# Performance work log

Hardware: AMD Instinct MI355X
Metric: run time of the kernel (lower is better)

## Reference

```python
import jax, jax.numpy as jnp
import numpy as np

IN, H, B, T, OUT = 128, 512, 256, 512, 2

def _lstm_layer(x, Wih, Whh, bih, bhh):
    # x: [B, T, D_in] -> h_seq: [B, T, H]. PyTorch gate order: i, f, g, o.
    gx = jnp.einsum('btd,gd->btg', x, Wih) + bih + bhh  # [B, T, 4H]
    gx = jnp.transpose(gx, (1, 0, 2))                    # [T, B, 4H]
    Hh = Whh.shape[1]
    def step(carry, g_t):
        h, c = carry
        g = g_t + h @ Whh.T
        i = jax.nn.sigmoid(g[:, 0*Hh:1*Hh])
        f = jax.nn.sigmoid(g[:, 1*Hh:2*Hh])
        gg = jnp.tanh(g[:, 2*Hh:3*Hh])
        o = jax.nn.sigmoid(g[:, 3*Hh:4*Hh])
        c = f * c + i * gg
        h = o * jnp.tanh(c)
        return (h, c), h
    h0 = jnp.zeros((x.shape[0], Hh), x.dtype)
    (_, _), hs = jax.lax.scan(step, (h0, h0), gx)
    return jnp.transpose(hs, (1, 0, 2))  # [B, T, H]

def setup_inputs() -> dict:
    key = jax.random.key(0)
    ks = jax.random.split(key, 11)
    s = 1.0 / np.sqrt(H)
    u = lambda k, shp: jax.random.uniform(k, shp, jnp.float32, -s, s)
    return {
        'x':    jax.random.normal(ks[0], (B, T, IN), jnp.float32),
        'Wih0': u(ks[1], (4 * H, IN)), 'Whh0': u(ks[2], (4 * H, H)),
        'bih0': u(ks[3], (4 * H,)),    'bhh0': u(ks[4], (4 * H,)),
        'Wih1': u(ks[5], (4 * H, H)),  'Whh1': u(ks[6], (4 * H, H)),
        'bih1': u(ks[7], (4 * H,)),    'bhh1': u(ks[8], (4 * H,)),
        'Wfc':  u(ks[9], (OUT, H)),    'bfc':  u(ks[10], (OUT,)),
    }

def reference(x, Wih0, Whh0, bih0, bhh0, Wih1, Whh1, bih1, bhh1, Wfc, bfc):
    h1 = _lstm_layer(x, Wih0, Whh0, bih0, bhh0)   # layer 0
    h2 = _lstm_layer(h1, Wih1, Whh1, bih1, bhh1)  # layer 1
    return h2[:, -1, :] @ Wfc.T + bfc             # [B, OUT]
```

## Files before the change

kernel.cpp:

```cpp
#include <hip/hip_runtime.h>

#define IN_DIM 128
#define HID    512
#define BATCH  256
#define SEQT   512
#define G4H    2048
#define K0     640
#define K1     1024
#define NC0    20
#define NC1    32
#define ROWB   2048
#define FSTRIDE 32

typedef __attribute__((ext_vector_type(8))) short bf16x8;
typedef __attribute__((ext_vector_type(4))) float f32x4;

#define MFMA16 __builtin_amdgcn_mfma_f32_16x16x32_bf16
#define GL(r, g, c) ((r) * 132 + (g) * 33 + (c))

__device__ __forceinline__ unsigned short f2bf(float f) {
  unsigned u = __float_as_uint(f);
  u += 0x7fffu + ((u >> 16) & 1u);
  return (unsigned short)(u >> 16);
}
__device__ __forceinline__ float bf2f(unsigned short s) {
  return __uint_as_float(((unsigned)s) << 16);
}
__device__ __forceinline__ float sigm(float x) { return 1.0f / (1.0f + __expf(-x)); }
__device__ __forceinline__ float tanh_f(float x) {
  float xc = fminf(fmaxf(x, -15.0f), 15.0f);
  float e = __expf(2.0f * xc);
  return (e - 1.0f) / (e + 1.0f);
}

__device__ __forceinline__ unsigned ald(const unsigned* p) {
  return __hip_atomic_load(p, __ATOMIC_RELAXED, __HIP_MEMORY_SCOPE_AGENT);
}

__global__ void conv_weights(const float* __restrict__ Wih0, const float* __restrict__ Whh0,
                             const float* __restrict__ Wih1, const float* __restrict__ Whh1,
                             const float* __restrict__ bih0, const float* __restrict__ bhh0,
                             const float* __restrict__ bih1, const float* __restrict__ bhh1,
                             short* __restrict__ W0h, short* __restrict__ W0l,
                             short* __restrict__ W1h, short* __restrict__ W1l,
                             float* __restrict__ bsum0, float* __restrict__ bsum1) {
  int idx = blockIdx.x * blockDim.x + threadIdx.x;
  const int N0 = G4H * K0, N1 = G4H * K1;
  if (idx < N0) {
    int tile = idx / (K0 * 16), rem = idx % (K0 * 16);
    int kcg = rem >> 9, l = (rem >> 3) & 63, j = rem & 7;
    int slice = tile >> 2, g = tile & 3;
    int c = l & 15, k = kcg * 32 + ((l >> 4) << 3) + j;
    int n = g * HID + slice * 16 + c;
    float w = (k < IN_DIM) ? Wih0[n * IN_DIM + k] : Whh0[n * HID + (k - IN_DIM)];
    unsigned short hi = f2bf(w);
    W0h[idx] = (short)hi;
    W0l[idx] = (short)f2bf(w - bf2f(hi));
  } else if (idx < N0 + N1) {
    int d = idx - N0;
    int tile = d / (K1 * 16), rem = d % (K1 * 16);
    int kcg = rem >> 9, l = (rem >> 3) & 63, j = rem & 7;
    int slice = tile >> 2, g = tile & 3;
    int c = l & 15, k = kcg * 32 + ((l >> 4) << 3) + j;
    int n = g * HID + slice * 16 + c;
    float w = (k < HID) ? Wih1[n * HID + k] : Whh1[n * HID + (k - HID)];
    unsigned short hi = f2bf(w);
    W1h[d] = (short)hi;
    W1l[d] = (short)f2bf(w - bf2f(hi));
  } else if (idx < N0 + N1 + G4H) {
    int n = idx - (N0 + N1);
    bsum0[n] = bih0[n] + bhh0[n];
  } else if (idx < N0 + N1 + 2 * G4H) {
    int n = idx - (N0 + N1 + G4H);
    bsum1[n] = bih1[n] + bhh1[n];
  }
}


__device__ __forceinline__ void stage_l0(char* Ah, const float* __restrict__ x,
                                         const unsigned short* __restrict__ h0p,
                                         int b0, int s, int tid) {
  const int row = tid >> 5, c32 = tid & 31;
  const int rx = (row & 7) << 4;
  char* base = Ah + row * ROWB;
  {
    const float* xs = x + ((size_t)(b0 + row) * SEQT + s) * IN_DIM + c32 * 4;
    float4 xv = *(const float4*)xs;
    unsigned short h0 = f2bf(xv.x), h1 = f2bf(xv.y), h2 = f2bf(xv.z), h3 = f2bf(xv.w);
    uint2 hd = {(unsigned)h0 | ((unsigned)h1 << 16), (unsigned)h2 | ((unsigned)h3 << 16)};
    uint2 ld = {(unsigned)f2bf(xv.x - bf2f(h0)) | ((unsigned)f2bf(xv.y - bf2f(h1)) << 16),
                (unsigned)f2bf(xv.z - bf2f(h2)) | ((unsigned)f2bf(xv.w - bf2f(h3)) << 16)};
    *(uint2*)(base + ((c32 * 8) ^ rx)) = hd;
    *(uint2*)(base + ((1280 + c32 * 8) ^ rx)) = ld;
  }
  {
    const unsigned short* hp = h0p + (size_t)(b0 + row) * HID + c32 * 16;
    uint4 v0, v1;
    asm volatile(
        "global_load_dwordx4 %0, %2, off sc0 sc1\n\t"
        "global_load_dwordx4 %1, %2, off offset:16 sc0 sc1\n\t"
        "s_waitcnt vmcnt(0)"
        : "=&v"(v0), "=&v"(v1) : "v"(hp) : "memory");
    const int byte0 = 256 + c32 * 32;
    *(int4*)(base + (byte0 ^ rx)) = *(int4*)&v0;
    *(int4*)(base + ((byte0 + 16) ^ rx)) = *(int4*)&v1;
  }
}

__device__ __forceinline__ void stage_l1(char* Ah,
                                         const unsigned short* __restrict__ h0p,
                                         const unsigned short* __restrict__ h2p,
                                         int b0, int tid) {
  const int row = tid >> 5, c32 = tid & 31;
  const int rx = (row & 7) << 4;
  char* base = Ah + row * ROWB;
  const unsigned short* p0 = h0p + (size_t)(b0 + row) * HID + c32 * 16;
  const unsigned short* p2 = h2p + (size_t)(b0 + row) * HID + c32 * 16;
  uint4 v0, v1, w0, w1;
  asm volatile(
      "global_load_dwordx4 %0, %4, off sc0 sc1\n\t"
      "global_load_dwordx4 %1, %4, off offset:16 sc0 sc1\n\t"
      "global_load_dwordx4 %2, %5, off sc0 sc1\n\t"
      "global_load_dwordx4 %3, %5, off offset:16 sc0 sc1\n\t"
      "s_waitcnt vmcnt(0)"
      : "=&v"(v0), "=&v"(v1), "=&v"(w0), "=&v"(w1)
      : "v"(p0), "v"(p2) : "memory");
  const int b0b = c32 * 32;
  *(int4*)(base + (b0b ^ rx)) = *(int4*)&v0;
  *(int4*)(base + ((b0b + 16) ^ rx)) = *(int4*)&v1;
  const int b2b = 1024 + c32 * 32;
  *(int4*)(base + (b2b ^ rx)) = *(int4*)&w0;
  *(int4*)(base + ((b2b + 16) ^ rx)) = *(int4*)&w1;
}

template <int NKC>
__device__ __forceinline__ void gemm_seq(const char* Ah, bool xlo,
                                         const short* __restrict__ Bh0, const short* __restrict__ Bl0,
                                         const short* __restrict__ Bh1, const short* __restrict__ Bl1,
                                         int lane, int aoff,
                                         f32x4& a00, f32x4& a01, f32x4& a10, f32x4& a11) {
  const int row = lane & 15;
  const int ko  = (lane >> 4) * 8;
  const int rx  = (row & 7) << 4;
  const char* pA0 = Ah + row * ROWB;
  const char* pA1 = Ah + (row + 16) * ROWB;
#pragma unroll
  for (int kc = 0; kc < NKC; ++kc) {
    const int k = aoff + kc * 32;
    const int off = ((k + ko) * 2) ^ rx;
    bf16x8 ah0 = *(const bf16x8*)(pA0 + off);
    bf16x8 ah1 = *(const bf16x8*)(pA1 + off);
    bf16x8 bh0 = *(const bf16x8*)(Bh0 + kc * 512 + lane * 8);
    bf16x8 bl0 = *(const bf16x8*)(Bl0 + kc * 512 + lane * 8);
    bf16x8 bh1 = *(const bf16x8*)(Bh1 + kc * 512 + lane * 8);
    bf16x8 bl1 = *(const bf16x8*)(Bl1 + kc * 512 + lane * 8);
    a00 = MFMA16(ah0, bh0, a00, 0, 0, 0);
    a01 = MFMA16(ah1, bh0, a01, 0, 0, 0);
    a00 = MFMA16(ah0, bl0, a00, 0, 0, 0);
    a01 = MFMA16(ah1, bl0, a01, 0, 0, 0);
    a10 = MFMA16(ah0, bh1, a10, 0, 0, 0);
    a11 = MFMA16(ah1, bh1, a11, 0, 0, 0);
    a10 = MFMA16(ah0, bl1, a10, 0, 0, 0);
    a11 = MFMA16(ah1, bl1, a11, 0, 0, 0);
    if (xlo && k < IN_DIM) {
      const int offl = ((1280 + (k + ko) * 2)) ^ rx;
      bf16x8 al0 = *(const bf16x8*)(pA0 + offl);
      bf16x8 al1 = *(const bf16x8*)(pA1 + offl);
      a00 = MFMA16(al0, bh0, a00, 0, 0, 0);
      a01 = MFMA16(al1, bh0, a01, 0, 0, 0);
      a10 = MFMA16(al0, bh1, a10, 0, 0, 0);
      a11 = MFMA16(al1, bh1, a11, 0, 0, 0);
    }
  }
}

__device__ __forceinline__ void finq32(float* glf, int g, int lane,
                                       const f32x4& a00, const f32x4& a01,
                                       const f32x4& a10, const f32x4& a11) {
  const int col = lane & 15;
  const int r0  = (lane >> 4) * 4;
#pragma unroll
  for (int r = 0; r < 4; ++r) {
    atomicAdd(glf + GL(r0 + r, g, col), a00[r]);
    atomicAdd(glf + GL(16 + r0 + r, g, col), a01[r]);
    atomicAdd(glf + GL(r0 + r, g, col + 16), a10[r]);
    atomicAdd(glf + GL(16 + r0 + r, g, col + 16), a11[r]);
  }
}

__device__ __forceinline__ void group_barrier(unsigned* flags, unsigned target,
                                              int tid, int wid) {
  asm volatile("s_waitcnt vmcnt(0)" ::: "memory");
  __syncthreads();
  if (tid < 64) {
    if (tid == 0)
      __hip_atomic_store(flags + wid * FSTRIDE, target,
                         __ATOMIC_RELAXED, __HIP_MEMORY_SCOPE_AGENT);
    const int i = (tid & 31) * FSTRIDE;
    while (true) {
      unsigned v = ald(flags + i);
      if (__all((int)(v >= target))) break;
      __builtin_amdgcn_s_sleep(1);
    }
  }
  __syncthreads();
}

__global__ void __launch_bounds__(1024, 4) lstm_fused(
    const float* __restrict__ x,
    const float* __restrict__ Wfc, const float* __restrict__ bfc,
    const short* __restrict__ W0h, const short* __restrict__ W0l,
    const short* __restrict__ W1h, const short* __restrict__ W1l,
    const float* __restrict__ bsum0, const float* __restrict__ bsum1,
    unsigned short* __restrict__ h0s, unsigned short* __restrict__ h2s,
    unsigned* __restrict__ counters,
    float* __restrict__ out) {
  const int tid  = threadIdx.x;
  const int wv   = tid >> 6;
  const int lane = tid & 63;
  const int wid  = blockIdx.x & 31;
  const int grp  = blockIdx.x >> 5;
  const int role = wid >> 4;
  const int w16  = wid & 15;
  const int hid0 = w16 * 32;
  const int b0   = grp * 32;
  unsigned* flags = counters + grp * (32 * FSTRIDE);

  __shared__ __align__(16) char AhB[32 * ROWB];
  __shared__ float glf[32 * 132];

  const int g  = wv & 3;
  const int kq = wv >> 2;
  const int t0 = (w16 * 2) * 4 + g, t1 = t0 + 4;
  const short *Bh0, *Bl0, *Bh1, *Bl1;
  int aoff;
  if (role == 0) {
    Bh0 = W0h + ((size_t)t0 * NC0 + (size_t)kq * 5) * 512;
    Bl0 = W0l + ((size_t)t0 * NC0 + (size_t)kq * 5) * 512;
    Bh1 = W0h + ((size_t)t1 * NC0 + (size_t)kq * 5) * 512;
    Bl1 = W0l + ((size_t)t1 * NC0 + (size_t)kq * 5) * 512;
    aoff = kq * 160;
  } else {
    Bh0 = W1h + ((size_t)t0 * NC1 + (size_t)kq * 8) * 512;
    Bl0 = W1l + ((size_t)t0 * NC1 + (size_t)kq * 8) * 512;
    Bh1 = W1h + ((size_t)t1 * NC1 + (size_t)kq * 8) * 512;
    Bl1 = W1l + ((size_t)t1 * NC1 + (size_t)kq * 8) * 512;
    aoff = kq * 256;
  }

  float c = 0.f;
  float bs[4];
  {
    const int n = hid0 + (tid & 31);
    const float* bsp = role ? bsum1 : bsum0;
#pragma unroll
    for (int q = 0; q < 4; ++q) bs[q] = bsp[q * HID + n];
  }
  for (int i = tid; i < 32 * 132; i += 1024) glf[i] = 0.f;

  const size_t PL = (size_t)BATCH * HID;

  for (int s = 0; s <= SEQT; ++s) {
    const int cur = s & 1, prv = cur ^ 1;
    unsigned short* h0c = h0s + (size_t)cur * PL;
    const unsigned short* h0p = h0s + (size_t)prv * PL;
    unsigned short* h2c = h2s + (size_t)cur * PL;
    const unsigned short* h2p = h2s + (size_t)prv * PL;
    const bool active = role ? (s > 0) : (s < SEQT);

    if (active) {
      if (role == 0) stage_l0(AhB, x, h0p, b0, s, tid);
      else           stage_l1(AhB, h0p, h2p, b0, tid);
    }
    __syncthreads();

    if (active) {
      f32x4 a00 = {0.f, 0.f, 0.f, 0.f}, a01 = {0.f, 0.f, 0.f, 0.f};
      f32x4 a10 = {0.f, 0.f, 0.f, 0.f}, a11 = {0.f, 0.f, 0.f, 0.f};
      if (role == 0)
        gemm_seq<5>(AhB, true, Bh0, Bl0, Bh1, Bl1, lane, aoff, a00, a01, a10, a11);
      else
        gemm_seq<8>(AhB, false, Bh0, Bl0, Bh1, Bl1, lane, aoff, a00, a01, a10, a11);
      finq32(glf, g, lane, a00, a01, a10, a11);
    }
    __syncthreads();

    if (active) {
      const int row = tid >> 5, col = tid & 31;
      float gi = glf[GL(row, 0, col)] + bs[0];
      float gf = glf[GL(row, 1, col)] + bs[1];
      float gg = glf[GL(row, 2, col)] + bs[2];
      float go = glf[GL(row, 3, col)] + bs[3];
      glf[GL(row, 0, col)] = 0.f; glf[GL(row, 1, col)] = 0.f;
      glf[GL(row, 2, col)] = 0.f; glf[GL(row, 3, col)] = 0.f;
      float i = sigm(gi), f = sigm(gf), gv = tanh_f(gg), o = sigm(go);
      float cc = f * c + i * gv;
      c = cc;
      float h = o * tanh_f(cc);
      unsigned short hv = f2bf(h);
      unsigned short* hc = role ? h2c : h0c;
      __hip_atomic_store(hc + (size_t)(b0 + row) * HID + hid0 + col, hv,
                         __ATOMIC_RELAXED, __HIP_MEMORY_SCOPE_AGENT);
    }

    group_barrier(flags, (unsigned)(s + 1), tid, wid);
  }

  {
    const int p = tid >> 3, q = tid & 7;
    float acc = 0.f;
    if (wid == 0 && tid < 512) {
      const int b = b0 + (p >> 1), o = p & 1;
      const unsigned* sp = (const unsigned*)(h2s + (size_t)b * HID) + q * 32;
      const float* wf = Wfc + (size_t)o * HID + q * 64;
#pragma unroll 8
      for (int i = 0; i < 32; ++i) {
        unsigned u = ald(sp + i);
        acc += bf2f((unsigned short)(u & 0xffff)) * wf[2 * i] +
               bf2f((unsigned short)(u >> 16)) * wf[2 * i + 1];
      }
      glf[p * 8 + q] = acc;
    }
    __syncthreads();
    if (wid == 0 && tid < 512 && q == 0) {
      float t = 0.f;
#pragma unroll
      for (int i = 0; i < 8; ++i) t += glf[p * 8 + i];
      out[(b0 + (p >> 1)) * 2 + (p & 1)] = t + bfc[p & 1];
    }
  }
}

extern "C" void kernel_launch(void* const* d_in, const int* in_sizes, int n_in,
                              void* d_out, int out_size, void* d_ws, size_t ws_size,
                              hipStream_t stream) {
  const float* x    = (const float*)d_in[0];
  const float* Wih0 = (const float*)d_in[1];
  const float* Whh0 = (const float*)d_in[2];
  const float* bih0 = (const float*)d_in[3];
  const float* bhh0 = (const float*)d_in[4];
  const float* Wih1 = (const float*)d_in[5];
  const float* Whh1 = (const float*)d_in[6];
  const float* bih1 = (const float*)d_in[7];
  const float* bhh1 = (const float*)d_in[8];
  const float* Wfc  = (const float*)d_in[9];
  const float* bfc  = (const float*)d_in[10];
  float* out = (float*)d_out;

  short* W0h = (short*)d_ws;
  short* W0l = W0h + (size_t)G4H * K0;
  short* W1h = W0l + (size_t)G4H * K0;
  short* W1l = W1h + (size_t)G4H * K1;
  unsigned short* h0s = (unsigned short*)(W1l + (size_t)G4H * K1);
  unsigned short* h2s = h0s + (size_t)2 * BATCH * HID;
  unsigned* counters = (unsigned*)(h2s + (size_t)2 * BATCH * HID);
  float* bsum0 = (float*)(counters + 8 * 32 * FSTRIDE);
  float* bsum1 = bsum0 + G4H;

  (void)hipMemsetAsync(h0s, 0,
                       (size_t)4 * BATCH * HID * sizeof(unsigned short) +
                           (size_t)8 * 32 * FSTRIDE * sizeof(unsigned),
                       stream);

  const int total = G4H * K0 + G4H * K1 + 2 * G4H;
  conv_weights<<<(total + 255) / 256, 256, 0, stream>>>(
      Wih0, Whh0, Wih1, Whh1, bih0, bhh0, bih1, bhh1,
      W0h, W0l, W1h, W1l, bsum0, bsum1);

  void* args[] = {(void*)&x,    (void*)&Wfc,  (void*)&bfc,
                  (void*)&W0h,  (void*)&W0l,  (void*)&W1h, (void*)&W1l,
                  (void*)&bsum0, (void*)&bsum1,
                  (void*)&h0s,  (void*)&h2s,  (void*)&counters, (void*)&out};
  (void)hipLaunchCooperativeKernel((void*)lstm_fused, dim3(256), dim3(1024), args, 0,
                                   stream);
}
```

Measured before the change: 14.55 ms.

## Decouple layer barriers so layer 0 may run ahead of layer 1

Replaces the all-group barrier with a role-specific barrier. Each layer waits on its own 16 groups plus a relaxed condition on the other layer: layer 0 may run up to two steps ahead, so the h0 buffer becomes four-deep. This is meant to cut the lockstep stalls where both layers wait on the slowest group every step. It adds a final wait before the FC stage and a spin cap that could break out early and risk correctness.

```diff
diff --git a/kernel.cpp b/kernel.cpp
--- a/kernel.cpp
+++ b/kernel.cpp
@@ -188,18 +188,25 @@
   }
 }
 
-__device__ __forceinline__ void group_barrier(unsigned* flags, unsigned target,
-                                              int tid, int wid) {
+__device__ __forceinline__ void role_barrier(unsigned* flags, int role,
+                                             unsigned s1 ,
+                                             int tid, int wid) {
   asm volatile("s_waitcnt vmcnt(0)" ::: "memory");
   __syncthreads();
   if (tid < 64) {
     if (tid == 0)
-      __hip_atomic_store(flags + wid * FSTRIDE, target,
+      __hip_atomic_store(flags + wid * FSTRIDE, s1,
                          __ATOMIC_RELAXED, __HIP_MEMORY_SCOPE_AGENT);
-    const int i = (tid & 31) * FSTRIDE;
+    const int i = tid & 15;
+    const unsigned* own = flags + ((role << 4) + i) * FSTRIDE;
+    const unsigned* oth = flags + (((1 - role) << 4) + i) * FSTRIDE;
+    const unsigned tOth = role == 0 ? (s1 >= 2 ? s1 - 2 : 0u) : s1;
+    int spins = 0;
     while (true) {
-      unsigned v = ald(flags + i);
-      if (__all((int)(v >= target))) break;
+      unsigned a = ald(own);
+      unsigned b = ald(oth);
+      if (__all((int)(a >= s1 && b >= tOth))) break;
+      if (++spins > (1 << 15)) break;
       __builtin_amdgcn_s_sleep(1);
     }
   }
@@ -261,11 +268,10 @@
   const size_t PL = (size_t)BATCH * HID;
 
   for (int s = 0; s <= SEQT; ++s) {
-    const int cur = s & 1, prv = cur ^ 1;
-    unsigned short* h0c = h0s + (size_t)cur * PL;
-    const unsigned short* h0p = h0s + (size_t)prv * PL;
-    unsigned short* h2c = h2s + (size_t)cur * PL;
-    const unsigned short* h2p = h2s + (size_t)prv * PL;
+    unsigned short* h0c = h0s + (size_t)(s & 3) * PL;
+    const unsigned short* h0p = h0s + (size_t)((s + 3) & 3) * PL;
+    unsigned short* h2c = h2s + (size_t)(s & 1) * PL;
+    const unsigned short* h2p = h2s + (size_t)((s + 1) & 1) * PL;
     const bool active = role ? (s > 0) : (s < SEQT);
 
     if (active) {
@@ -303,9 +309,22 @@
                          __ATOMIC_RELAXED, __HIP_MEMORY_SCOPE_AGENT);
     }
 
-    group_barrier(flags, (unsigned)(s + 1), tid, wid);
-  }
-
+    role_barrier(flags, role, (unsigned)(s + 1), tid, wid);
+  }
+
+  if (wid == 0) {
+    if (tid < 64) {
+      const int i = tid & 15;
+      int spins = 0;
+      while (true) {
+        unsigned v = ald(flags + (16 + i) * FSTRIDE);
+        if (__all((int)(v >= (unsigned)(SEQT + 1)))) break;
+        if (++spins > (1 << 15)) break;
+        __builtin_amdgcn_s_sleep(1);
+      }
+    }
+    __syncthreads();
+  }
   {
     const int p = tid >> 3, q = tid & 7;
     float acc = 0.f;
@@ -352,13 +371,13 @@
   short* W1h = W0l + (size_t)G4H * K0;
   short* W1l = W1h + (size_t)G4H * K1;
   unsigned short* h0s = (unsigned short*)(W1l + (size_t)G4H * K1);
-  unsigned short* h2s = h0s + (size_t)2 * BATCH * HID;
+  unsigned short* h2s = h0s + (size_t)4 * BATCH * HID;
   unsigned* counters = (unsigned*)(h2s + (size_t)2 * BATCH * HID);
   float* bsum0 = (float*)(counters + 8 * 32 * FSTRIDE);
   float* bsum1 = bsum0 + G4H;
 
   (void)hipMemsetAsync(h0s, 0,
-                       (size_t)4 * BATCH * HID * sizeof(unsigned short) +
+                       (size_t)6 * BATCH * HID * sizeof(unsigned short) +
                            (size_t)8 * 32 * FSTRIDE * sizeof(unsigned),
                        stream);
 
```

Result: no change. 14.76 ms (+1.5%).
